# Kernel optimization log

Measured on AMD Instinct MI355X. Metric: run time of the kernel, lower is better.

## Reference

```python
import jax, jax.numpy as jnp
import numpy as np

N_NODES = 100000
N_EDGES = 1600000
IN_CH = 128
HID = 128   # 2 * out_channels
OUT = 64


def setup_inputs() -> dict:
    key = jax.random.key(0)
    ks = jax.random.split(key, 5)
    x = jax.random.normal(ks[0], (N_NODES, IN_CH), dtype=jnp.float32)
    edge_index = jax.random.randint(ks[1], (2, N_EDGES), 0, N_NODES, dtype=jnp.int64)
    # Glorot-ish init for the two GCN weight matrices
    W1 = jax.random.normal(ks[2], (IN_CH, HID), dtype=jnp.float32) / np.sqrt(IN_CH)
    b1 = jnp.zeros((HID,), dtype=jnp.float32)
    W2 = jax.random.normal(ks[3], (HID, OUT), dtype=jnp.float32) / np.sqrt(HID)
    b2 = jnp.zeros((OUT,), dtype=jnp.float32)
    return {"x": x, "edge_index": edge_index, "W1": W1, "b1": b1, "W2": W2, "b2": b2}


def _gcn_conv(x, W, b, src, dst, coef, n):
    # Standard GCNConv: D^{-1/2} (A + I) D^{-1/2} X W + b
    xw = x @ W                                   # [N, F_out]
    msg = xw[src] * coef[:, None]                # gather + scale  [E+N, F_out]
    agg = jax.ops.segment_sum(msg, dst, num_segments=n)  # scatter-add [N, F_out]
    return agg + b


def reference(x, edge_index, W1, b1, W2, b2):
    n = x.shape[0]
    loops = jnp.arange(n, dtype=edge_index.dtype)
    src = jnp.concatenate([edge_index[0], loops])  # add self loops
    dst = jnp.concatenate([edge_index[1], loops])
    deg = jax.ops.segment_sum(jnp.ones_like(src, dtype=x.dtype), dst, num_segments=n)
    dinv = jnp.where(deg > 0, jax.lax.rsqrt(deg), 0.0)
    coef = dinv[src] * dinv[dst]                  # symmetric normalization per edge

    h = _gcn_conv(x, W1, b1, src, dst, coef, n)
    h = jax.nn.relu(h)                            # non_linearity=True
    # F.normalize(p=2, dim=-1) with eps clamp 1e-12; dropout inactive (eval mode)
    h = h / jnp.maximum(jnp.linalg.norm(h, axis=-1, keepdims=True), 1e-12)
    return _gcn_conv(h, W2, b2, src, dst, coef, n)
```

## Files before the change

kernel.cpp:

```cpp
#include <hip/hip_runtime.h>
#include <hip/hip_bf16.h>


#define IN_CH 128
#define HID 128
#define OUT_CH 64
#define NBLK 128
#define MAXNB 1568

typedef unsigned int uint_t;
typedef unsigned short ushort_t;

__device__ __forceinline__ ushort_t f32_to_bf16_rn(float f) {
    uint_t u = __float_as_uint(f);
    u = (u + 0x7fffu + ((u >> 16) & 1u)) >> 16;
    return (ushort_t)u;
}
__device__ __forceinline__ float bf16lo_to_f32(uint_t u) { return __uint_as_float(u << 16); }
__device__ __forceinline__ float bf16hi_to_f32(uint_t u) { return __uint_as_float(u & 0xffff0000u); }

__global__ __launch_bounds__(256) void hist_kernel(const int* __restrict__ dst, int E,
                                                   int chunk, int NB,
                                                   int* __restrict__ blk_cnt) {
    __shared__ int hist[MAXNB];
    int tid = threadIdx.x;
    int blk = blockIdx.x;
    for (int b = tid; b < NB; b += 256) hist[b] = 0;
    __syncthreads();
    int start = blk * chunk;
    int end = start + chunk; if (end > E) end = E;
    int e = start + tid;
    for (; e + 768 < end; e += 1024) {
        int d0 = dst[e], d1 = dst[e + 256], d2 = dst[e + 512], d3 = dst[e + 768];
        atomicAdd(&hist[d0 >> 6], 1);
        atomicAdd(&hist[d1 >> 6], 1);
        atomicAdd(&hist[d2 >> 6], 1);
        atomicAdd(&hist[d3 >> 6], 1);
    }
    for (; e < end; e += 256) atomicAdd(&hist[dst[e] >> 6], 1);
    __syncthreads();
    for (int b = tid; b < NB; b += 256) blk_cnt[blk * NB + b] = hist[b];
}

__global__ __launch_bounds__(256) void btot_kernel(const int* __restrict__ blk_cnt,
                                                   int NB, int* __restrict__ btot) {
    int b = blockIdx.x * 256 + threadIdx.x;
    if (b < NB) {
        int sum = 0;
        #pragma unroll 8
        for (int blk = 0; blk < NBLK; blk++) sum += blk_cnt[blk * NB + b];
        btot[b] = sum;
    }
}

__global__ __launch_bounds__(256) void scan_kernel(const int* __restrict__ btot, int NB,
                                                   int* __restrict__ bucket_base,
                                                   int* __restrict__ row_start,
                                                   int n, int E) {
    __shared__ int sdata[256];
    __shared__ int carryS;
    int tid = threadIdx.x;
    if (tid == 0) carryS = 0;
    __syncthreads();
    int nchunks = (NB + 255) / 256;
    for (int c = 0; c < nchunks; c++) {
        int i = c * 256 + tid;
        int v = (i < NB) ? btot[i] : 0;
        sdata[tid] = v;
        __syncthreads();
        for (int off = 1; off < 256; off <<= 1) {
            int t = (tid >= off) ? sdata[tid - off] : 0;
            __syncthreads();
            sdata[tid] += t;
            __syncthreads();
        }
        if (i < NB) bucket_base[i] = carryS + sdata[tid] - v;
        __syncthreads();
        if (tid == 0) carryS += sdata[255];
        __syncthreads();
    }
    if (tid == 0) {
        bucket_base[NB] = E;
        row_start[n] = E;
    }
}

__global__ __launch_bounds__(256) void colscan_kernel(const int* __restrict__ blk_cnt,
                                                      const int* __restrict__ bucket_base,
                                                      int NB, int* __restrict__ blk_start) {
    __shared__ int tile[NBLK][16];
    int tid = threadIdx.x;
    int b0 = blockIdx.x * 16;
    for (int idx = tid; idx < NBLK * 16; idx += 256) {
        int blk = idx >> 4, b = idx & 15;
        if (b0 + b < NB) tile[blk][b] = blk_cnt[blk * NB + b0 + b];
    }
    __syncthreads();
    if (tid < 16 && b0 + tid < NB) {
        int running = bucket_base[b0 + tid];
        for (int blk = 0; blk < NBLK; blk++) {
            int t = tile[blk][tid];
            tile[blk][tid] = running;
            running += t;
        }
    }
    __syncthreads();
    for (int idx = tid; idx < NBLK * 16; idx += 256) {
        int blk = idx >> 4, b = idx & 15;
        if (b0 + b < NB) blk_start[blk * NB + b0 + b] = tile[blk][b];
    }
}

__global__ __launch_bounds__(256) void scatter_kernel(const int* __restrict__ src,
                                                      const int* __restrict__ dst,
                                                      int E, int chunk, int NB,
                                                      const int* __restrict__ blk_start,
                                                      uint_t* __restrict__ pairs) {
    __shared__ int cur[MAXNB];
    int tid = threadIdx.x;
    int blk = blockIdx.x;
    for (int b = tid; b < NB; b += 256) cur[b] = blk_start[blk * NB + b];
    __syncthreads();
    int start = blk * chunk;
    int end = start + chunk; if (end > E) end = E;
    int e = start + tid;
    for (; e + 768 < end; e += 1024) {
        int d0 = dst[e], d1 = dst[e + 256], d2 = dst[e + 512], d3 = dst[e + 768];
        int s0 = src[e], s1 = src[e + 256], s2 = src[e + 512], s3 = src[e + 768];
        int p0 = atomicAdd(&cur[d0 >> 6], 1);
        int p1 = atomicAdd(&cur[d1 >> 6], 1);
        int p2 = atomicAdd(&cur[d2 >> 6], 1);
        int p3 = atomicAdd(&cur[d3 >> 6], 1);
        pairs[p0] = (uint_t)s0 | ((uint_t)(d0 & 63) << 26);
        pairs[p1] = (uint_t)s1 | ((uint_t)(d1 & 63) << 26);
        pairs[p2] = (uint_t)s2 | ((uint_t)(d2 & 63) << 26);
        pairs[p3] = (uint_t)s3 | ((uint_t)(d3 & 63) << 26);
    }
    for (; e < end; e += 256) {
        int d = dst[e], s = src[e];
        int p = atomicAdd(&cur[d >> 6], 1);
        pairs[p] = (uint_t)s | ((uint_t)(d & 63) << 26);
    }
}

__global__ __launch_bounds__(256) void fine_fill_kernel(const uint_t* __restrict__ pairs,
                                                        const int* __restrict__ bucket_base,
                                                        int* __restrict__ row_start,
                                                        float* __restrict__ dinv,
                                                        int* __restrict__ csr_src,
                                                        int n) {
    __shared__ int cnt64[64];
    __shared__ int cur[64];
    int b = blockIdx.x;
    int node0 = b << 6;
    int tid = threadIdx.x;
    if (tid < 64) cnt64[tid] = 0;
    __syncthreads();
    int start = bucket_base[b];
    int end = bucket_base[b + 1];
    int e = start + tid;
    for (; e + 768 < end; e += 1024) {
        uint_t u0 = pairs[e], u1 = pairs[e + 256], u2 = pairs[e + 512], u3 = pairs[e + 768];
        atomicAdd(&cnt64[u0 >> 26], 1);
        atomicAdd(&cnt64[u1 >> 26], 1);
        atomicAdd(&cnt64[u2 >> 26], 1);
        atomicAdd(&cnt64[u3 >> 26], 1);
    }
    for (; e < end; e += 256) atomicAdd(&cnt64[pairs[e] >> 26], 1);
    __syncthreads();
    if (tid < 64) {
        int c = cnt64[tid];
        int v = c;
        #pragma unroll
        for (int off = 1; off < 64; off <<= 1) {
            int u = __shfl_up(v, off, 64);
            if (tid >= off) v += u;
        }
        int excl = start + v - c;
        if (node0 + tid < n) {
            row_start[node0 + tid] = excl;
            dinv[node0 + tid] = rsqrtf((float)(c + 1));
        }
        cur[tid] = excl;
    }
    __syncthreads();
    e = start + tid;
    for (; e + 768 < end; e += 1024) {
        uint_t u0 = pairs[e], u1 = pairs[e + 256], u2 = pairs[e + 512], u3 = pairs[e + 768];
        int p0 = atomicAdd(&cur[u0 >> 26], 1);
        int p1 = atomicAdd(&cur[u1 >> 26], 1);
        int p2 = atomicAdd(&cur[u2 >> 26], 1);
        int p3 = atomicAdd(&cur[u3 >> 26], 1);
        csr_src[p0] = (int)(u0 & 0x3FFFFFFu);
        csr_src[p1] = (int)(u1 & 0x3FFFFFFu);
        csr_src[p2] = (int)(u2 & 0x3FFFFFFu);
        csr_src[p3] = (int)(u3 & 0x3FFFFFFu);
    }
    for (; e < end; e += 256) {
        uint_t u = pairs[e];
        int p = atomicAdd(&cur[u >> 26], 1);
        csr_src[p] = (int)(u & 0x3FFFFFFu);
    }
}

template <int NCOL, bool BF16_IN>
__global__ __launch_bounds__(256, 3) void gemm_kernel(const void* __restrict__ Xv,
                                                      const float* __restrict__ W,
                                                      const float* __restrict__ rowscale,
                                                      ushort_t* __restrict__ Y, int nrows) {
    constexpr int K = 128;
    constexpr int KT = 32;
    constexpr int CPL = NCOL / 64;
    __shared__ __align__(16) float Xs[64 * K];
    __shared__ __align__(16) float Ws[KT * NCOL];

    int tid = threadIdx.x;
    int wave = tid >> 6;
    int lane = tid & 63;
    int rowBase = blockIdx.x * 64;
    int r0 = wave * 16;

    if (BF16_IN) {
        const uint_t* X = (const uint_t*)Xv;
        for (int j = tid; j < 64 * (K / 2); j += 256) {
            int r = j >> 6;
            int c = j & 63;
            int gr = rowBase + r;
            uint_t u = (gr < nrows) ? X[(size_t)gr * (K / 2) + c] : 0u;
            Xs[r * K + 2 * c]     = bf16lo_to_f32(u);
            Xs[r * K + 2 * c + 1] = bf16hi_to_f32(u);
        }
    } else {
        const float4* X4 = (const float4*)Xv;
        float4* Xs4 = (float4*)Xs;
        for (int j = tid; j < 64 * (K / 4); j += 256) {
            int r = j >> 5;
            int gr = rowBase + r;
            float4 v = make_float4(0.f, 0.f, 0.f, 0.f);
            if (gr < nrows) v = X4[(size_t)gr * (K / 4) + (j & 31)];
            Xs4[j] = v;
        }
    }

    float acc[16][CPL];
    #pragma unroll
    for (int r = 0; r < 16; r++)
        #pragma unroll
        for (int c = 0; c < CPL; c++) acc[r][c] = 0.f;

    #pragma unroll 1
    for (int kt = 0; kt < K; kt += KT) {
        __syncthreads();
        {
            float4* Ws4 = (float4*)Ws;
            const float4* W4 = (const float4*)W;
            for (int j = tid; j < KT * (NCOL / 4); j += 256)
                Ws4[j] = W4[(size_t)kt * (NCOL / 4) + j];
        }
        __syncthreads();
        #pragma unroll 2
        for (int k4 = 0; k4 < KT; k4 += 4) {
            float wv[4][CPL];
            #pragma unroll
            for (int kk = 0; kk < 4; kk++)
                #pragma unroll
                for (int c = 0; c < CPL; c++)
                    wv[kk][c] = Ws[(k4 + kk) * NCOL + lane * CPL + c];
            #pragma unroll
            for (int r = 0; r < 16; r++) {
                float4 xv = *(const float4*)&Xs[(r0 + r) * K + kt + k4];
                #pragma unroll
                for (int c = 0; c < CPL; c++) {
                    acc[r][c] = fmaf(xv.x, wv[0][c], acc[r][c]);
                    acc[r][c] = fmaf(xv.y, wv[1][c], acc[r][c]);
                    acc[r][c] = fmaf(xv.z, wv[2][c], acc[r][c]);
                    acc[r][c] = fmaf(xv.w, wv[3][c], acc[r][c]);
                }
            }
        }
    }

    #pragma unroll
    for (int r = 0; r < 16; r++) {
        int gr = rowBase + r0 + r;
        if (gr < nrows) {
            float rs = rowscale[gr];
            if (CPL == 2) {
                uint_t u = (uint_t)f32_to_bf16_rn(acc[r][0] * rs) |
                           ((uint_t)f32_to_bf16_rn(acc[r][CPL - 1] * rs) << 16);
                ((uint_t*)(Y + (size_t)gr * NCOL))[lane] = u;
            } else {
                Y[(size_t)gr * NCOL + lane] = f32_to_bf16_rn(acc[r][0] * rs);
            }
        }
    }
}

__global__ __launch_bounds__(256) void agg1_kernel(const ushort_t* __restrict__ xw,
                                                   const int* __restrict__ csr_src,
                                                   const int* __restrict__ row_start,
                                                   const float* __restrict__ dinv,
                                                   const float* __restrict__ b1,
                                                   ushort_t* __restrict__ h, int n) {
    int wid = (blockIdx.x * 256 + threadIdx.x) >> 6;
    int lane = threadIdx.x & 63;
    if (wid >= n) return;
    int i = wid;
    float di = dinv[i];
    int e0 = row_start[i], e1 = row_start[i + 1];
    uint_t su = ((const uint_t*)(xw + (size_t)i * HID))[lane];
    float ax = bf16lo_to_f32(su), ay = bf16hi_to_f32(su);
    int e = e0;
    for (; e + 8 <= e1; e += 8) {
        int s[8];
        #pragma unroll
        for (int j = 0; j < 8; j++) s[j] = csr_src[e + j];
        uint_t v[8];
        #pragma unroll
        for (int j = 0; j < 8; j++)
            v[j] = ((const uint_t*)(xw + (size_t)s[j] * HID))[lane];
        #pragma unroll
        for (int j = 0; j < 8; j++) {
            ax += bf16lo_to_f32(v[j]);
            ay += bf16hi_to_f32(v[j]);
        }
    }
    if (e < e1) {
        int last = e1 - 1;
        int s[8];
        #pragma unroll
        for (int j = 0; j < 8; j++) {
            int idx = e + j;
            s[j] = csr_src[idx <= last ? idx : last];
        }
        uint_t v[8];
        #pragma unroll
        for (int j = 0; j < 8; j++)
            v[j] = ((const uint_t*)(xw + (size_t)s[j] * HID))[lane];
        #pragma unroll
        for (int j = 0; j < 8; j++) {
            float c = (e + j <= last) ? 1.0f : 0.0f;
            ax = fmaf(bf16lo_to_f32(v[j]), c, ax);
            ay = fmaf(bf16hi_to_f32(v[j]), c, ay);
        }
    }
    ax = fmaf(ax, di, b1[lane * 2]);
    ay = fmaf(ay, di, b1[lane * 2 + 1]);
    ax = fmaxf(ax, 0.f);
    ay = fmaxf(ay, 0.f);
    float ss = ax * ax + ay * ay;
    #pragma unroll
    for (int m = 32; m >= 1; m >>= 1) ss += __shfl_xor(ss, m, 64);
    float scale = 1.0f / fmaxf(sqrtf(ss), 1e-12f);
    uint_t u = (uint_t)f32_to_bf16_rn(ax * scale) |
               ((uint_t)f32_to_bf16_rn(ay * scale) << 16);
    ((uint_t*)(h + (size_t)i * HID))[lane] = u;
}

__global__ __launch_bounds__(256) void agg2_kernel(const ushort_t* __restrict__ hw,
                                                   const int* __restrict__ csr_src,
                                                   const int* __restrict__ row_start,
                                                   const float* __restrict__ dinv,
                                                   const float* __restrict__ b2,
                                                   float* __restrict__ out, int n) {
    int wid = (blockIdx.x * 256 + threadIdx.x) >> 6;
    int lane = threadIdx.x & 63;
    int i = wid * 2 + (lane >> 5);
    int l = lane & 31;
    if (i >= n) return;
    float di = dinv[i];
    uint_t su = ((const uint_t*)(hw + (size_t)i * OUT_CH))[l];
    float ax = bf16lo_to_f32(su), ay = bf16hi_to_f32(su);
    int e0 = row_start[i], e1 = row_start[i + 1];
    int e = e0;
    for (; e + 8 <= e1; e += 8) {
        int s[8];
        #pragma unroll
        for (int j = 0; j < 8; j++) s[j] = csr_src[e + j];
        uint_t v[8];
        #pragma unroll
        for (int j = 0; j < 8; j++)
            v[j] = ((const uint_t*)(hw + (size_t)s[j] * OUT_CH))[l];
        #pragma unroll
        for (int j = 0; j < 8; j++) {
            ax += bf16lo_to_f32(v[j]);
            ay += bf16hi_to_f32(v[j]);
        }
    }
    if (e < e1) {
        int last = e1 - 1;
        int s[8];
        #pragma unroll
        for (int j = 0; j < 8; j++) {
            int idx = e + j;
            s[j] = csr_src[idx <= last ? idx : last];
        }
        uint_t v[8];
        #pragma unroll
        for (int j = 0; j < 8; j++)
            v[j] = ((const uint_t*)(hw + (size_t)s[j] * OUT_CH))[l];
        #pragma unroll
        for (int j = 0; j < 8; j++) {
            float c = (e + j <= last) ? 1.0f : 0.0f;
            ax = fmaf(bf16lo_to_f32(v[j]), c, ax);
            ay = fmaf(bf16hi_to_f32(v[j]), c, ay);
        }
    }
    ax = fmaf(ax, di, b2[l * 2]);
    ay = fmaf(ay, di, b2[l * 2 + 1]);
    ((float2*)(out + (size_t)i * OUT_CH))[l] = make_float2(ax, ay);
}

extern "C" void kernel_launch(void* const* d_in, const int* in_sizes, int n_in,
                              void* d_out, int out_size, void* d_ws, size_t ws_size,
                              hipStream_t stream) {
    const float* x  = (const float*)d_in[0];
    const int*   ei = (const int*)d_in[1];
    const float* W1 = (const float*)d_in[2];
    const float* b1 = (const float*)d_in[3];
    const float* W2 = (const float*)d_in[4];
    const float* b2 = (const float*)d_in[5];
    float* out = (float*)d_out;

    const int N = in_sizes[0] / IN_CH;
    const int E = in_sizes[1] / 2;
    const int* src = ei;
    const int* dst = ei + E;
    const int NB = (N + 63) / 64;
    const int chunk = (E + NBLK - 1) / NBLK;

    char* base = (char*)d_ws;
    size_t off = 0;
    auto alloc = [&](size_t bytes) -> void* {
        void* p = base + off;
        off = (off + bytes + 255) & ~(size_t)255;
        return p;
    };
    int*      blk_cnt     = (int*)alloc((size_t)NBLK * NB * 4);
    int*      blk_start   = (int*)alloc((size_t)NBLK * NB * 4);
    int*      btot        = (int*)alloc((size_t)NB * 4);
    int*      bucket_base = (int*)alloc((size_t)(NB + 1) * 4);
    int*      row_start   = (int*)alloc((size_t)(N + 1) * 4);
    float*    dinv        = (float*)alloc((size_t)N * 4);
    int*      csr_src     = (int*)alloc((size_t)E * 4);
    uint_t*   pairs       = (uint_t*)alloc((size_t)E * 4);
    ushort_t* xw          = (ushort_t*)alloc((size_t)N * HID * 2);
    ushort_t* h           = (ushort_t*)alloc((size_t)N * HID * 2);
    ushort_t* hw          = (ushort_t*)alloc((size_t)N * OUT_CH * 2);
    (void)ws_size;

    hist_kernel<<<NBLK, 256, 0, stream>>>(dst, E, chunk, NB, blk_cnt);
    btot_kernel<<<(NB + 255) / 256, 256, 0, stream>>>(blk_cnt, NB, btot);
    scan_kernel<<<1, 256, 0, stream>>>(btot, NB, bucket_base, row_start, N, E);
    colscan_kernel<<<(NB + 15) / 16, 256, 0, stream>>>(blk_cnt, bucket_base, NB, blk_start);
    scatter_kernel<<<NBLK, 256, 0, stream>>>(src, dst, E, chunk, NB, blk_start, pairs);
    fine_fill_kernel<<<NB, 256, 0, stream>>>(pairs, bucket_base, row_start, dinv,
                                             csr_src, N);

    gemm_kernel<128, false><<<(N + 63) / 64, 256, 0, stream>>>(x, W1, dinv, xw, N);
    agg1_kernel<<<(N * 64 + 255) / 256, 256, 0, stream>>>(xw, csr_src, row_start,
                                                          dinv, b1, h, N);
    gemm_kernel<64, true><<<(N + 63) / 64, 256, 0, stream>>>(h, W2, dinv, hw, N);
    int waves2 = (N + 1) / 2;
    agg2_kernel<<<(waves2 * 64 + 255) / 256, 256, 0, stream>>>(hw, csr_src, row_start,
                                                               dinv, b2, out, N);
}
```

Measured before the change: 360.1 us.

## Replace FP32 SIMT GEMMs with split-bf16 MFMA matrix-core GEMMs

Replaces both dense feature-transform GEMMs, which used FP32 FMAs staged through LDS, with MFMA 16x16x32 bf16 instructions. To keep near-fp32 accuracy, W and the fp32 input are each split into high and low bf16 parts and three MFMA products are accumulated. A small preprocessing kernel writes the transposed, split weights. Shared-memory tiling is dropped, so operands are read straight from global memory or cache, which may cost bandwidth in exchange for much higher compute throughput.

New measurement: 346.8 us. 3.7% less time.

```diff
diff --git a/kernel.cpp b/kernel.cpp
--- a/kernel.cpp
+++ b/kernel.cpp
@@ -10,6 +10,8 @@
 
 typedef unsigned int uint_t;
 typedef unsigned short ushort_t;
+typedef __attribute__((ext_vector_type(8))) short bf16x8;
+typedef __attribute__((ext_vector_type(4))) float f32x4;
 
 __device__ __forceinline__ ushort_t f32_to_bf16_rn(float f) {
     uint_t u = __float_as_uint(f);
@@ -203,95 +205,97 @@
     }
 }
 
-template <int NCOL, bool BF16_IN>
-__global__ __launch_bounds__(256, 3) void gemm_kernel(const void* __restrict__ Xv,
-                                                      const float* __restrict__ W,
-                                                      const float* __restrict__ rowscale,
-                                                      ushort_t* __restrict__ Y, int nrows) {
-    constexpr int K = 128;
-    constexpr int KT = 32;
-    constexpr int CPL = NCOL / 64;
-    __shared__ __align__(16) float Xs[64 * K];
-    __shared__ __align__(16) float Ws[KT * NCOL];
+__global__ __launch_bounds__(256) void wsplit_kernel(const float* __restrict__ W1,
+                                                     const float* __restrict__ W2,
+                                                     ushort_t* __restrict__ w1h,
+                                                     ushort_t* __restrict__ w1l,
+                                                     ushort_t* __restrict__ w2h,
+                                                     ushort_t* __restrict__ w2l) {
+    int idx = blockIdx.x * 256 + threadIdx.x;
+    const int tot1 = 128 * 128;
+    const int tot = tot1 + 64 * 128;
+    if (idx >= tot) return;
+    float v;
+    ushort_t* ph;
+    ushort_t* pl;
+    int o;
+    if (idx < tot1) {
+        int c = idx >> 7, k = idx & 127;
+        v = W1[k * 128 + c];
+        ph = w1h; pl = w1l; o = idx;
+    } else {
+        int j = idx - tot1;
+        int c = j >> 7, k = j & 127;
+        v = W2[k * 64 + c];
+        ph = w2h; pl = w2l; o = j;
+    }
+    ushort_t h = f32_to_bf16_rn(v);
+    float hv = __uint_as_float((uint_t)h << 16);
+    ph[o] = h;
+    pl[o] = f32_to_bf16_rn(v - hv);
+}
+
+template <int NCOL, bool F32_IN>
+__global__ __launch_bounds__(256) void mfma_gemm_kernel(const void* __restrict__ Xv,
+                                                        const ushort_t* __restrict__ Wth,
+                                                        const ushort_t* __restrict__ Wtl,
+                                                        const float* __restrict__ rowscale,
+                                                        ushort_t* __restrict__ Y, int n) {
+    constexpr int NT = NCOL / 16;
+    const float* X = (const float*)Xv;
+    const ushort_t* Hb = (const ushort_t*)Xv;
 
     int tid = threadIdx.x;
     int wave = tid >> 6;
     int lane = tid & 63;
-    int rowBase = blockIdx.x * 64;
-    int r0 = wave * 16;
-
-    if (BF16_IN) {
-        const uint_t* X = (const uint_t*)Xv;
-        for (int j = tid; j < 64 * (K / 2); j += 256) {
-            int r = j >> 6;
-            int c = j & 63;
-            int gr = rowBase + r;
-            uint_t u = (gr < nrows) ? X[(size_t)gr * (K / 2) + c] : 0u;
-            Xs[r * K + 2 * c]     = bf16lo_to_f32(u);
-            Xs[r * K + 2 * c + 1] = bf16hi_to_f32(u);
-        }
-    } else {
-        const float4* X4 = (const float4*)Xv;
-        float4* Xs4 = (float4*)Xs;
-        for (int j = tid; j < 64 * (K / 4); j += 256) {
-            int r = j >> 5;
-            int gr = rowBase + r;
-            float4 v = make_float4(0.f, 0.f, 0.f, 0.f);
-            if (gr < nrows) v = X4[(size_t)gr * (K / 4) + (j & 31)];
-            Xs4[j] = v;
-        }
-    }
-
-    float acc[16][CPL];
+    int q = lane >> 4;
+    int r16 = lane & 15;
+    int rowBase = blockIdx.x * 64 + wave * 16;
+    int arow = rowBase + r16;
+    if (arow > n - 1) arow = n - 1;
+
+    f32x4 acc[NT];
     #pragma unroll
-    for (int r = 0; r < 16; r++)
-        #pragma unroll
-        for (int c = 0; c < CPL; c++) acc[r][c] = 0.f;
-
-    #pragma unroll 1
-    for (int kt = 0; kt < K; kt += KT) {
-        __syncthreads();
-        {
-            float4* Ws4 = (float4*)Ws;
-            const float4* W4 = (const float4*)W;
-            for (int j = tid; j < KT * (NCOL / 4); j += 256)
-                Ws4[j] = W4[(size_t)kt * (NCOL / 4) + j];
-        }
-        __syncthreads();
-        #pragma unroll 2
-        for (int k4 = 0; k4 < KT; k4 += 4) {
-            float wv[4][CPL];
+    for (int t = 0; t < NT; t++) acc[t] = (f32x4){0.f, 0.f, 0.f, 0.f};
+
+    #pragma unroll
+    for (int ks = 0; ks < 4; ks++) {
+        int k0 = ks * 32 + q * 8;
+        bf16x8 ah, al = {};
+        if (F32_IN) {
+            const float4* xr = (const float4*)(X + (size_t)arow * 128 + k0);
+            float4 p0 = xr[0], p1 = xr[1];
+            float v[8] = {p0.x, p0.y, p0.z, p0.w, p1.x, p1.y, p1.z, p1.w};
             #pragma unroll
-            for (int kk = 0; kk < 4; kk++)
-                #pragma unroll
-                for (int c = 0; c < CPL; c++)
-                    wv[kk][c] = Ws[(k4 + kk) * NCOL + lane * CPL + c];
+            for (int j = 0; j < 8; j++) {
+                ushort_t hb = f32_to_bf16_rn(v[j]);
+                float hv = __uint_as_float((uint_t)hb << 16);
+                ah[j] = (short)hb;
+                al[j] = (short)f32_to_bf16_rn(v[j] - hv);
+            }
+        } else {
+            ah = *(const bf16x8*)(Hb + (size_t)arow * 128 + k0);
+        }
+        #pragma unroll
+        for (int t = 0; t < NT; t++) {
+            size_t wo = (size_t)(t * 16 + r16) * 128 + k0;
+            bf16x8 bh = *(const bf16x8*)(Wth + wo);
+            bf16x8 bl = *(const bf16x8*)(Wtl + wo);
+            acc[t] = __builtin_amdgcn_mfma_f32_16x16x32_bf16(ah, bh, acc[t], 0, 0, 0);
+            acc[t] = __builtin_amdgcn_mfma_f32_16x16x32_bf16(ah, bl, acc[t], 0, 0, 0);
+            if (F32_IN)
+                acc[t] = __builtin_amdgcn_mfma_f32_16x16x32_bf16(al, bh, acc[t], 0, 0, 0);
+        }
+    }
+
+    #pragma unroll
+    for (int rr = 0; rr < 4; rr++) {
+        int row = rowBase + q * 4 + rr;
+        if (row < n) {
+            float rs = rowscale[row];
             #pragma unroll
-            for (int r = 0; r < 16; r++) {
-                float4 xv = *(const float4*)&Xs[(r0 + r) * K + kt + k4];
-                #pragma unroll
-                for (int c = 0; c < CPL; c++) {
-                    acc[r][c] = fmaf(xv.x, wv[0][c], acc[r][c]);
-                    acc[r][c] = fmaf(xv.y, wv[1][c], acc[r][c]);
-                    acc[r][c] = fmaf(xv.z, wv[2][c], acc[r][c]);
-                    acc[r][c] = fmaf(xv.w, wv[3][c], acc[r][c]);
-                }
-            }
-        }
-    }
-
-    #pragma unroll
-    for (int r = 0; r < 16; r++) {
-        int gr = rowBase + r0 + r;
-        if (gr < nrows) {
-            float rs = rowscale[gr];
-            if (CPL == 2) {
-                uint_t u = (uint_t)f32_to_bf16_rn(acc[r][0] * rs) |
-                           ((uint_t)f32_to_bf16_rn(acc[r][CPL - 1] * rs) << 16);
-                ((uint_t*)(Y + (size_t)gr * NCOL))[lane] = u;
-            } else {
-                Y[(size_t)gr * NCOL + lane] = f32_to_bf16_rn(acc[r][0] * rs);
-            }
+            for (int t = 0; t < NT; t++)
+                Y[(size_t)row * NCOL + t * 16 + r16] = f32_to_bf16_rn(acc[t][rr] * rs);
         }
     }
 }
@@ -447,7 +451,14 @@
     ushort_t* xw          = (ushort_t*)alloc((size_t)N * HID * 2);
     ushort_t* h           = (ushort_t*)alloc((size_t)N * HID * 2);
     ushort_t* hw          = (ushort_t*)alloc((size_t)N * OUT_CH * 2);
+    ushort_t* w1h         = (ushort_t*)alloc((size_t)128 * 128 * 2);
+    ushort_t* w1l         = (ushort_t*)alloc((size_t)128 * 128 * 2);
+    ushort_t* w2h         = (ushort_t*)alloc((size_t)64 * 128 * 2);
+    ushort_t* w2l         = (ushort_t*)alloc((size_t)64 * 128 * 2);
     (void)ws_size;
+
+    wsplit_kernel<<<(128 * 128 + 64 * 128 + 255) / 256, 256, 0, stream>>>(
+        W1, W2, w1h, w1l, w2h, w2l);
 
     hist_kernel<<<NBLK, 256, 0, stream>>>(dst, E, chunk, NB, blk_cnt);
     btot_kernel<<<(NB + 255) / 256, 256, 0, stream>>>(blk_cnt, NB, btot);
@@ -457,10 +468,12 @@
     fine_fill_kernel<<<NB, 256, 0, stream>>>(pairs, bucket_base, row_start, dinv,
                                              csr_src, N);
 
-    gemm_kernel<128, false><<<(N + 63) / 64, 256, 0, stream>>>(x, W1, dinv, xw, N);
+    mfma_gemm_kernel<128, true><<<(N + 63) / 64, 256, 0, stream>>>(
+        x, w1h, w1l, dinv, xw, N);
     agg1_kernel<<<(N * 64 + 255) / 256, 256, 0, stream>>>(xw, csr_src, row_start,
                                                           dinv, b1, h, N);
-    gemm_kernel<64, true><<<(N + 63) / 64, 256, 0, stream>>>(h, W2, dinv, hw, N);
+    mfma_gemm_kernel<64, false><<<(N + 63) / 64, 256, 0, stream>>>(
+        h, w2h, w2l, dinv, hw, N);
     int waves2 = (N + 1) / 2;
     agg2_kernel<<<(waves2 * 64 + 255) / 256, 256, 0, stream>>>(hw, csr_src, row_start,
                                                                dinv, b2, out, N);
```
